# Performance work log

Hardware: AMD Instinct MI355X
Metric: run time of the kernel (lower is better)

## Reference

```python
import jax, jax.numpy as jnp
import numpy as np

B, L, HID, NH = 1, 2048, 3072, 24
HD = HID // NH          # 128
MLP = HID * 4           # 12288


def _layernorm(x, eps=1e-6):
    # LayerNorm without affine (pre_norm)
    mu = jnp.mean(x, axis=-1, keepdims=True)
    var = jnp.mean(jnp.square(x - mu), axis=-1, keepdims=True)
    return (x - mu) * jax.lax.rsqrt(var + eps)


def _rmsnorm(x, w):
    # torch.nn.RMSNorm with eps=None -> finfo(dtype).eps
    eps = jnp.finfo(x.dtype).eps
    ms = jnp.mean(jnp.square(x), axis=-1, keepdims=True)
    return x * jax.lax.rsqrt(ms + eps) * w


def _apply_rope(x, pe):
    # x: (B, L, H, D); pe: (B, 1, L, D//2, 2, 2)
    b, l, h, d = x.shape
    x_ = x.astype(jnp.float32).reshape(b, l, h, d // 2, 1, 2)
    f = pe[:, :, :, None]                       # (B,1,L,1,D//2,2,2)
    out = f[..., 0] * x_[..., 0] + f[..., 1] * x_[..., 1]
    return out.reshape(b, l, h, d).astype(x.dtype)


def setup_inputs() -> dict:
    key = jax.random.key(0)
    ks = jax.random.split(key, 16)
    s = 0.02
    # pe as proper 2x2 rotation matrices (EmbedND output structure)
    theta = jax.random.uniform(ks[0], (L, HD // 2), minval=0.0, maxval=2.0 * np.pi)
    cos, sin = jnp.cos(theta), jnp.sin(theta)
    rot = jnp.stack([jnp.stack([cos, -sin], -1), jnp.stack([sin, cos], -1)], -2)
    pe = rot[None, None].astype(jnp.float32)    # (1,1,L,HD//2,2,2)
    rnd = lambda k, shp: jax.random.normal(k, shp, jnp.float32)
    return {
        "x": rnd(ks[1], (B, L, HID)),
        "vec": rnd(ks[2], (B, HID)),
        "pe": pe,
        "w_mod": rnd(ks[3], (HID, 3 * HID)) * s,
        "b_mod": rnd(ks[4], (3 * HID,)) * s,
        "w_qkv": rnd(ks[5], (HID, 3 * HID)) * s,
        "b_qkv": rnd(ks[6], (3 * HID,)) * s,
        "w_fc1": rnd(ks[7], (HID, MLP)) * s,
        "b_fc1": rnd(ks[8], (MLP,)) * s,
        "w_fc2": rnd(ks[9], (MLP, HID)) * s,
        "b_fc2": rnd(ks[10], (HID,)) * s,
        "w_out": rnd(ks[11], (HID, HID)) * s,
        "b_out": rnd(ks[12], (HID,)) * s,
        "norm_q_w": jnp.ones((HD,), jnp.float32),
        "norm_k_w": jnp.ones((HD,), jnp.float32),
    }


def reference(x, vec, pe, w_mod, b_mod, w_qkv, b_qkv, w_fc1, b_fc1,
              w_fc2, b_fc2, w_out, b_out, norm_q_w, norm_k_w):
    # modulation: AWQ linear on silu(vec)
    mod = jax.nn.silu(vec) @ w_mod + b_mod            # (B, 3*HID)
    shift, scale, gate = jnp.split(mod[:, None, :], 3, axis=-1)
    x_mod = _layernorm(x) * (1.0 + scale) + shift      # (B, L, HID)

    # qkv projection (SVDQ linear, dequantized math == dense GEMM)
    qkv = x_mod @ w_qkv + b_qkv
    q, k, v = jnp.split(qkv, 3, axis=-1)
    q = _rmsnorm(q.reshape(B, L, NH, HD), norm_q_w)
    k = _rmsnorm(k.reshape(B, L, NH, HD), norm_k_w)
    q = _apply_rope(q, pe)
    k = _apply_rope(k, pe)
    v = v.reshape(B, L, NH, HD)

    # scaled dot-product attention
    scores = jnp.einsum("blhd,bmhd->bhlm", q, k) / jnp.sqrt(jnp.float32(HD))
    probs = jax.nn.softmax(scores, axis=-1)
    attn = jnp.einsum("bhlm,bmhd->blhd", probs, v).reshape(B, L, HID)

    # parallel MLP branch
    mlp = jax.nn.gelu(x_mod @ w_fc1 + b_fc1, approximate=True)
    mlp = mlp @ w_fc2 + b_fc2

    out = attn @ w_out + b_out + mlp
    return x + gate * out
```

## Files before the change

### kernel.cpp

```cpp
#include <hip/hip_runtime.h>
#include <hip/hip_bf16.h>
#include <stdint.h>


typedef __bf16 bf16;
typedef bf16 bf16x2 __attribute__((ext_vector_type(2)));
typedef bf16 bf16x4 __attribute__((ext_vector_type(4)));
typedef bf16 bf16x8 __attribute__((ext_vector_type(8)));
typedef float f32x4 __attribute__((ext_vector_type(4)));

#define L_SEQ 2048
#define HIDD  3072
#define NHH   24
#define HDD   128
#define MLPD  12288
#define N3Q   9216

struct PB { bf16* p[4]; };

__device__ __forceinline__ void gload_lds16(const bf16* g, bf16* l) {
  __builtin_amdgcn_global_load_lds(
      (const __attribute__((address_space(1))) unsigned int*)g,
      (__attribute__((address_space(3))) unsigned int*)l, 16, 0, 0);
}

__device__ __forceinline__ float gelu_tanh(float x) {
  float z = 0.7978845608028654f * (x + 0.044715f * x * x * x);
  float t = 1.f - 2.f / (__expf(2.f * z) + 1.f);
  return 0.5f * x * (1.f + t);
}

__global__ __launch_bounds__(256) void mod_partial(
    const float* __restrict__ vec, const float* __restrict__ w_mod,
    float* __restrict__ part) {
  __shared__ float sv[256];
  int y = blockIdx.y;
  int i0 = y * 256;
  {
    float xv = vec[i0 + threadIdx.x];
    sv[threadIdx.x] = xv / (1.f + __expf(-xv));
  }
  __syncthreads();
  int j = blockIdx.x * 256 + threadIdx.x;
  float acc = 0.f;
#pragma unroll 8
  for (int i = 0; i < 256; ++i)
    acc += sv[i] * w_mod[(size_t)(i0 + i) * N3Q + j];
  part[y * N3Q + j] = acc;
}

__global__ __launch_bounds__(256) void mod_reduce(
    const float* __restrict__ part, const float* __restrict__ b_mod,
    float* __restrict__ mod) {
  int j = blockIdx.x * 256 + threadIdx.x;
  float s = b_mod[j];
#pragma unroll
  for (int p = 0; p < 12; ++p) s += part[p * N3Q + j];
  mod[j] = s;
}

__global__ __launch_bounds__(256) void ln_mod_k(
    const float* __restrict__ x, const float* __restrict__ mod,
    bf16* __restrict__ xm) {
  __shared__ float sb[4];
  int l = blockIdx.x, t = threadIdx.x;
  const float* xr = x + (size_t)l * HIDD;
  float4 v[3];
  float s = 0.f;
#pragma unroll
  for (int p = 0; p < 3; ++p) {
    v[p] = *(const float4*)(xr + p * 1024 + t * 4);
    s += v[p].x + v[p].y + v[p].z + v[p].w;
  }
#pragma unroll
  for (int o = 32; o >= 1; o >>= 1) s += __shfl_xor(s, o);
  if (!(t & 63)) sb[t >> 6] = s;
  __syncthreads();
  float mean = (sb[0] + sb[1] + sb[2] + sb[3]) * (1.f / HIDD);
  __syncthreads();
  float vs = 0.f;
#pragma unroll
  for (int p = 0; p < 3; ++p) {
    float a = v[p].x - mean, b = v[p].y - mean, c = v[p].z - mean,
          d = v[p].w - mean;
    vs += a * a + b * b + c * c + d * d;
  }
#pragma unroll
  for (int o = 32; o >= 1; o >>= 1) vs += __shfl_xor(vs, o);
  if (!(t & 63)) sb[t >> 6] = vs;
  __syncthreads();
  float var = (sb[0] + sb[1] + sb[2] + sb[3]) * (1.f / HIDD);
  float rs = rsqrtf(var + 1e-6f);
#pragma unroll
  for (int p = 0; p < 3; ++p) {
    int j = p * 1024 + t * 4;
    float4 sc = *(const float4*)(mod + HIDD + j);
    float4 sh = *(const float4*)(mod + j);
    bf16x4 o;
    o[0] = (bf16)((v[p].x - mean) * rs * (1.f + sc.x) + sh.x);
    o[1] = (bf16)((v[p].y - mean) * rs * (1.f + sc.y) + sh.y);
    o[2] = (bf16)((v[p].z - mean) * rs * (1.f + sc.z) + sh.z);
    o[3] = (bf16)((v[p].w - mean) * rs * (1.f + sc.w) + sh.w);
    *(bf16x4*)(xm + (size_t)l * HIDD + j) = o;
  }
}

__global__ __launch_bounds__(256) void convT(
    const float* __restrict__ src, bf16* __restrict__ dst, int K, int N) {
  __shared__ bf16 tl[64 * 73];
  int n0 = blockIdx.x * 64, k0 = blockIdx.y * 64;
  int t = threadIdx.x;
#pragma unroll
  for (int p = 0; p < 4; ++p) {
    int idx = p * 256 + t;
    int kr = idx >> 4, c4 = (idx & 15) << 2;
    float4 v = *(const float4*)(src + (size_t)(k0 + kr) * N + n0 + c4);
    bf16x4 b;
    b[0] = (bf16)v.x; b[1] = (bf16)v.y; b[2] = (bf16)v.z; b[3] = (bf16)v.w;
    *(bf16x4*)(tl + kr * 73 + c4) = b;
  }
  __syncthreads();
#pragma unroll
  for (int p = 0; p < 2; ++p) {
    int idx = p * 256 + t;
    int nr = idx >> 3, c = idx & 7;
    bf16x8 o;
#pragma unroll
    for (int j = 0; j < 8; ++j) o[j] = tl[(c * 8 + j) * 73 + nr];
    *(bf16x8*)(dst + (size_t)(n0 + nr) * K + k0 + c * 8) = o;
  }
}

template <int EPI>
__global__ __launch_bounds__(512, 2) void gemm256(
    const bf16* __restrict__ A, const bf16* __restrict__ BT,
    const float* __restrict__ bias, int lda, int klen, int gy, int gz,
    PB dst, bf16* __restrict__ o1, const bf16* __restrict__ BT2,
    const bf16* __restrict__ BT3, float* __restrict__ o32) {
  __shared__ bf16 LA[2][2][8192];
  __shared__ bf16 LB[2][2][8192];
  const int tid = threadIdx.x;
  const int w = tid >> 6, lane = tid & 63;
  const int wm = w >> 2, wn = w & 3;
  const int g = lane >> 4, r16 = lane & 15;
  const int hb = wn >> 1, brow = (wn & 1) * 64;

  const int nwg = 8 * gy * gz;
  int id = (int)blockIdx.x;
  int sw = (id & 7) * (nwg >> 3) + (id >> 3);
  const int bx = sw & 7;
  const int rem = sw >> 3;
  const int by = rem % gy;
  const int bz = rem / gy;

  const int row0 = bx * 256, col0 = by * 256;

  const int s_r = tid >> 3, s_c = tid & 7;
  const int swzoff = (s_c ^ (s_r & 7)) << 3;

  int lda_eff = lda;
  const bf16* Abase = A;
  const bf16* Bbase = BT;
  size_t kb2 = 0;
  int bcol = col0;
  if (EPI == 2) {
    if (by >= 36)      { Bbase = BT3; bcol = col0 - 9216; }
    else if (by >= 32) { Bbase = BT2; bcol = col0 - 8192; }
  } else if (EPI == 3) {
    if (bz != 0) {
      lda_eff = MLPD;
      Abase = BT3;
      Bbase = BT2;
      kb2 = (size_t)(bz - 1) * 3072;
    }
  }
  const bf16* gA = Abase + (size_t)(row0 + s_r) * lda_eff + kb2 + swzoff;
  const bf16* gB = Bbase + (size_t)(bcol + s_r) * lda_eff + kb2 + swzoff;
  const int wofs = w * 512;

#define STG_A(buf, h, t)                                                       \
  do {                                                                         \
    gload_lds16(gA + (size_t)((h) * 128) * lda_eff + (size_t)(t) * 64,         \
                &LA[buf][h][wofs]);                                            \
    gload_lds16(gA + (size_t)((h) * 128 + 64) * lda_eff + (size_t)(t) * 64,    \
                &LA[buf][h][4096 + wofs]);                                     \
  } while (0)
#define STG_B(buf, h, t)                                                       \
  do {                                                                         \
    gload_lds16(gB + (size_t)((h) * 128) * lda_eff + (size_t)(t) * 64,         \
                &LB[buf][h][wofs]);                                            \
    gload_lds16(gB + (size_t)((h) * 128 + 64) * lda_eff + (size_t)(t) * 64,    \
                &LB[buf][h][4096 + wofs]);                                     \
  } while (0)
#define SB0() __builtin_amdgcn_sched_barrier(0)
#define RD_A4(DST, LAP, MB)                                                    \
  _Pragma("unroll") for (int m_ = 0; m_ < 4; ++m_)                             \
  _Pragma("unroll") for (int kk_ = 0; kk_ < 2; ++kk_)                          \
      DST[m_][kk_] = *(const bf16x8*)((LAP) + (((MB) + m_) * 16 + r16) * 64 +  \
                                      (((kk_ * 4 + g) ^ (r16 & 7)) << 3));
#define RD_B2(DST, LBP, NB)                                                    \
  _Pragma("unroll") for (int n_ = 0; n_ < 2; ++n_)                             \
  _Pragma("unroll") for (int kk_ = 0; kk_ < 2; ++kk_)                          \
      DST[n_][kk_] = *(const bf16x8*)(                                         \
          (LBP) + (brow + ((NB) + n_) * 16 + r16) * 64 +                       \
          (((kk_ * 4 + g) ^ (r16 & 7)) << 3));
#define QUAD(AF, BF, MB, NB)                                                   \
  do {                                                                         \
    __builtin_amdgcn_s_setprio(1);                                             \
    _Pragma("unroll") for (int kk_ = 0; kk_ < 2; ++kk_)                        \
    _Pragma("unroll") for (int m_ = 0; m_ < 4; ++m_)                           \
    _Pragma("unroll") for (int n_ = 0; n_ < 2; ++n_)                           \
        acc[(MB) + m_][(NB) + n_] = __builtin_amdgcn_mfma_f32_16x16x32_bf16(   \
            AF[m_][kk_], BF[n_][kk_], acc[(MB) + m_][(NB) + n_], 0, 0, 0);     \
    __builtin_amdgcn_s_setprio(0);                                             \
  } while (0)

#define GROUP(TB, T1, T2)                                                      \
  do {                                                                         \
    const bf16* la = &LA[TB][wm][0];                                           \
    const bf16* lb = &LB[TB][hb][0];                                           \
    bf16x8 aL[4][2], aH[4][2], bL[2][2], bH[2][2];                             \
                                           \
    RD_A4(aL, la, 0);                                                          \
    RD_B2(bL, lb, 0);                                                          \
    if ((T1) < nk) STG_B(TB ^ 1, 1, T1);                                       \
    __builtin_amdgcn_s_barrier();                                              \
    SB0();                                                                     \
    QUAD(aL, bL, 0, 0);                                                        \
    __builtin_amdgcn_s_barrier();                                              \
                      \
    RD_A4(aH, la, 4);                                                          \
    __builtin_amdgcn_s_barrier();                                              \
    SB0();                                                                     \
    QUAD(aH, bL, 4, 0);                                                        \
    __builtin_amdgcn_s_barrier();                                              \
     \
    RD_B2(bH, lb, 2);                                                          \
    if ((T2) < nk) { STG_A(TB, 0, T2); STG_A(TB, 1, T2); }                     \
    __builtin_amdgcn_s_barrier();                                              \
    SB0();                                                                     \
    QUAD(aL, bH, 0, 2);                                                        \
    __builtin_amdgcn_s_barrier();                                              \
       \
    if ((T2) < nk) {                                                           \
      STG_B(TB, 0, T2);                                                        \
      asm volatile("s_waitcnt vmcnt(6)" ::: "memory");                         \
    } else {                                                                   \
      asm volatile("s_waitcnt vmcnt(0)" ::: "memory");                         \
    }                                                                          \
    __builtin_amdgcn_s_barrier();                                              \
    SB0();                                                                     \
    QUAD(aH, bH, 4, 2);                                                        \
    __builtin_amdgcn_s_barrier();                                              \
  } while (0)

  f32x4 acc[8][4] = {};
  const int nk = klen >> 6;

  STG_A(0, 0, 0); STG_A(0, 1, 0); STG_B(0, 0, 0); STG_B(0, 1, 0);
  STG_A(1, 0, 1); STG_A(1, 1, 1); STG_B(1, 0, 1);
  asm volatile("s_waitcnt vmcnt(6)" ::: "memory");
  __builtin_amdgcn_s_barrier();

  for (int t = 0; t < nk; t += 2) {
    GROUP(0, t + 1, t + 2);
    GROUP(1, t + 2, t + 3);
  }
#undef STG_A
#undef STG_B
#undef SB0
#undef RD_A4
#undef RD_B2
#undef QUAD
#undef GROUP

  if (EPI == 2 && by < 36) {
    bf16* dp = dst.p[0];
#pragma unroll
    for (int m = 0; m < 8; ++m) {
      int row = row0 + wm * 128 + m * 16 + g * 4;
#pragma unroll
      for (int n = 0; n < 4; ++n) {
        int col = col0 + wn * 64 + n * 16 + r16;
#pragma unroll
        for (int r = 0; r < 4; ++r)
          dp[(size_t)(row + r) * N3Q + col] = (bf16)acc[m][n][r];
      }
    }
  } else if (EPI == 2) {
    bf16* dp = o1;
#pragma unroll
    for (int m = 0; m < 8; ++m) {
      int row = row0 + wm * 128 + m * 16 + g * 4;
#pragma unroll
      for (int n = 0; n < 4; ++n) {
        int col = col0 - 9216 + wn * 64 + n * 16 + r16;
        float bv = bias[col];
#pragma unroll
        for (int r = 0; r < 4; ++r)
          dp[(size_t)(row + r) * MLPD + col] = (bf16)gelu_tanh(acc[m][n][r] + bv);
      }
    }
  } else if (EPI == 3 && bz == 0) {
#pragma unroll
    for (int m = 0; m < 8; ++m) {
      int row = row0 + wm * 128 + m * 16 + g * 4;
#pragma unroll
      for (int n = 0; n < 4; ++n) {
        int col = col0 + wn * 64 + n * 16 + r16;
#pragma unroll
        for (int r = 0; r < 4; ++r)
          o32[(size_t)(row + r) * HIDD + col] = acc[m][n][r];
      }
    }
  } else {
    bf16* dp = dst.p[bz - 1];
#pragma unroll
    for (int m = 0; m < 8; ++m) {
      int row = row0 + wm * 128 + m * 16 + g * 4;
#pragma unroll
      for (int n = 0; n < 4; ++n) {
        int col = col0 + wn * 64 + n * 16 + r16;
#pragma unroll
        for (int r = 0; r < 4; ++r)
          dp[(size_t)(row + r) * HIDD + col] = (bf16)acc[m][n][r];
      }
    }
  }
}

__global__ __launch_bounds__(256) void qknorm_rope_k(
    const bf16* __restrict__ P, const float* __restrict__ b_qkv,
    const float* __restrict__ pe, const float* __restrict__ qw,
    const float* __restrict__ kw, bf16* __restrict__ qb,
    bf16* __restrict__ kb) {
  int t = threadIdx.x, lane = t & 63, w = t >> 6;
  int pair = blockIdx.x * 4 + w;
  int h = pair % NHH, l = pair / NHH;
  size_t qi = (size_t)l * N3Q + h * HDD + 2 * lane;
  size_t ob = (size_t)l * HIDD + h * HDD + 2 * lane;
  float4 f = *(const float4*)(pe + (size_t)l * 256 + lane * 4);
  float2 wq = *(const float2*)(qw + 2 * lane);
  float2 wk = *(const float2*)(kw + 2 * lane);
  {
    bf16x2 a = *(const bf16x2*)(P + qi);
    float2 bq = *(const float2*)(b_qkv + h * HDD + 2 * lane);
    float x0 = (float)a[0] + bq.x;
    float x1 = (float)a[1] + bq.y;
    float ss = x0 * x0 + x1 * x1;
#pragma unroll
    for (int o = 32; o >= 1; o >>= 1) ss += __shfl_xor(ss, o);
    float rs = rsqrtf(ss * (1.f / HDD) + 1.1920929e-7f);
    x0 *= rs * wq.x; x1 *= rs * wq.y;
    const float qs = 0.08838834764831845f;
    bf16x2 ov;
    ov[0] = (bf16)((f.x * x0 + f.y * x1) * qs);
    ov[1] = (bf16)((f.z * x0 + f.w * x1) * qs);
    *(bf16x2*)(qb + ob) = ov;
  }
  {
    bf16x2 a = *(const bf16x2*)(P + qi + HIDD);
    float2 bk = *(const float2*)(b_qkv + HIDD + h * HDD + 2 * lane);
    float x0 = (float)a[0] + bk.x;
    float x1 = (float)a[1] + bk.y;
    float ss = x0 * x0 + x1 * x1;
#pragma unroll
    for (int o = 32; o >= 1; o >>= 1) ss += __shfl_xor(ss, o);
    float rs = rsqrtf(ss * (1.f / HDD) + 1.1920929e-7f);
    x0 *= rs * wk.x; x1 *= rs * wk.y;
    bf16x2 ov;
    ov[0] = (bf16)(f.x * x0 + f.y * x1);
    ov[1] = (bf16)(f.z * x0 + f.w * x1);
    *(bf16x2*)(kb + ob) = ov;
  }
}

__global__ __launch_bounds__(256) void vtrans_k(
    const bf16* __restrict__ P, const float* __restrict__ b_qkv,
    bf16* __restrict__ vt) {
  __shared__ bf16 tl[128 * 128];
  int t = threadIdx.x, lt = blockIdx.x, h = blockIdx.y;
#pragma unroll
  for (int p = 0; p < 8; ++p) {
    int idx = p * 256 + t;
    int i = idx >> 4, c = idx & 15;
    size_t gi = (size_t)(lt * 128 + i) * N3Q + 2 * HIDD + h * HDD + c * 8;
    bf16x8 a = *(const bf16x8*)(P + gi);
    bf16x8 val;
#pragma unroll
    for (int e = 0; e < 8; ++e)
      val[e] = (bf16)((float)a[e] + b_qkv[2 * HIDD + h * HDD + c * 8 + e]);
    *(bf16x8*)(tl + i * 128 + ((c ^ (i & 15)) << 3)) = val;
  }
  __syncthreads();
#pragma unroll
  for (int p = 0; p < 8; ++p) {
    int idx = p * 256 + t;
    int j = idx >> 4, i8 = (idx & 15) << 3;
    bf16x8 o;
#pragma unroll
    for (int e = 0; e < 8; ++e) {
      int row = i8 + e;
      o[e] = tl[row * 128 + ((((j >> 3) ^ (row & 15)) << 3) | (j & 7))];
    }
    *(bf16x8*)(vt + ((size_t)h * HDD + j) * L_SEQ + lt * 128 + i8) = o;
  }
}

__global__ __launch_bounds__(256) void attn_k(
    const bf16* __restrict__ q, const bf16* __restrict__ k,
    const bf16* __restrict__ vt, bf16* __restrict__ out) {
  __shared__ bf16 Ks[64 * 128];
  __shared__ bf16 Vs[128 * 64];
  __shared__ bf16 Ps[4][16 * 72];
  int tid = threadIdx.x, lane = tid & 63, w = tid >> 6;
  int g = lane >> 4, r16 = lane & 15;
  int qt = blockIdx.x, h = blockIdx.y;
  int qbase = qt * 64 + w * 16;

  bf16x8 qreg[4];
  const bf16* qrow = q + (size_t)(qbase + r16) * HIDD + h * HDD;
#pragma unroll
  for (int c = 0; c < 4; ++c) qreg[c] = *(const bf16x8*)(qrow + c * 32 + g * 8);

  f32x4 acc[8] = {};
  float m_run = -3.0e38f, l_run = 0.f;
  bf16* ps = &Ps[w][0];

  for (int kv0 = 0; kv0 < L_SEQ; kv0 += 64) {
    __syncthreads();
#pragma unroll
    for (int p = 0; p < 4; ++p) {
      int ci = p * 256 + tid;
      {
        int rr = ci >> 4, cc = ci & 15;
        gload_lds16(k + (size_t)(kv0 + rr) * HIDD + h * HDD +
                        ((cc ^ (rr & 15)) << 3),
                    Ks + ((p * 4 + w) << 9));
      }
      {
        int rr = ci >> 3, cc = ci & 7;
        gload_lds16(vt + ((size_t)h * HDD + rr) * L_SEQ + kv0 +
                        ((cc ^ (rr & 7)) << 3),
                    Vs + ((p * 4 + w) << 9));
      }
    }
    __syncthreads();

    f32x4 st[4] = {};
#pragma unroll
    for (int m4 = 0; m4 < 4; ++m4) {
#pragma unroll
      for (int c = 0; c < 4; ++c) {
        int rr = m4 * 16 + r16;
        bf16x8 kf =
            *(const bf16x8*)(Ks + rr * 128 + (((c * 4 + g) ^ (rr & 15)) << 3));
        st[m4] =
            __builtin_amdgcn_mfma_f32_16x16x32_bf16(kf, qreg[c], st[m4], 0, 0, 0);
      }
    }
    float cmax = -3.0e38f;
#pragma unroll
    for (int m4 = 0; m4 < 4; ++m4)
#pragma unroll
      for (int r = 0; r < 4; ++r) cmax = fmaxf(cmax, st[m4][r]);
    cmax = fmaxf(cmax, __shfl_xor(cmax, 16));
    cmax = fmaxf(cmax, __shfl_xor(cmax, 32));
    float m_new = fmaxf(m_run, cmax);
    float corr = __expf(m_run - m_new);
    float psum = 0.f;
#pragma unroll
    for (int m4 = 0; m4 < 4; ++m4) {
      bf16x4 pk;
#pragma unroll
      for (int r = 0; r < 4; ++r) {
        float pv = __expf(st[m4][r] - m_new);
        psum += pv;
        pk[r] = (bf16)pv;
      }
      *(bf16x4*)(ps + r16 * 72 + m4 * 16 + g * 4) = pk;
    }
    psum += __shfl_xor(psum, 16);
    psum += __shfl_xor(psum, 32);
    l_run = l_run * corr + psum;
    m_run = m_new;
    float corr_r[4];
#pragma unroll
    for (int r = 0; r < 4; ++r) corr_r[r] = __shfl(corr, g * 4 + r);
#pragma unroll
    for (int nt = 0; nt < 8; ++nt)
#pragma unroll
      for (int r = 0; r < 4; ++r) acc[nt][r] *= corr_r[r];
#pragma unroll
    for (int ks = 0; ks < 2; ++ks) {
      bf16x8 pf = *(const bf16x8*)(ps + r16 * 72 + ks * 32 + g * 8);
#pragma unroll
      for (int nt = 0; nt < 8; ++nt) {
        int rr = nt * 16 + r16;
        bf16x8 vf =
            *(const bf16x8*)(Vs + rr * 64 + (((ks * 4 + g) ^ (rr & 7)) << 3));
        acc[nt] = __builtin_amdgcn_mfma_f32_16x16x32_bf16(pf, vf, acc[nt], 0, 0, 0);
      }
    }
  }
  float inv = 1.f / l_run;
  float inv_r[4];
#pragma unroll
  for (int r = 0; r < 4; ++r) inv_r[r] = __shfl(inv, g * 4 + r);
#pragma unroll
  for (int nt = 0; nt < 8; ++nt)
#pragma unroll
    for (int r = 0; r < 4; ++r)
      out[(size_t)(qbase + g * 4 + r) * HIDD + h * HDD + nt * 16 + r16] =
          (bf16)(acc[nt][r] * inv_r[r]);
}

__global__ __launch_bounds__(256) void final_k(
    const float* __restrict__ x, PB ps, const float* __restrict__ mod,
    const float* __restrict__ b_out, const float* __restrict__ b_fc2,
    float* __restrict__ out) {
  int l = blockIdx.x, t = threadIdx.x;
#pragma unroll
  for (int p = 0; p < 3; ++p) {
    int c = p * 1024 + t * 4;
    size_t idx = (size_t)l * HIDD + c;
    float4 xv = *(const float4*)(x + idx);
    float4 gv = *(const float4*)(mod + 2 * HIDD + c);
    float4 bo = *(const float4*)(b_out + c);
    float4 bf = *(const float4*)(b_fc2 + c);
    float4 da = *(const float4*)(out + idx);
    float a0 = da.x + bo.x + bf.x, a1 = da.y + bo.y + bf.y;
    float a2 = da.z + bo.z + bf.z, a3 = da.w + bo.w + bf.w;
#pragma unroll
    for (int i = 0; i < 4; ++i) {
      bf16x4 v = *(const bf16x4*)(ps.p[i] + idx);
      a0 += (float)v[0]; a1 += (float)v[1];
      a2 += (float)v[2]; a3 += (float)v[3];
    }
    float4 o;
    o.x = xv.x + gv.x * a0;
    o.y = xv.y + gv.y * a1;
    o.z = xv.z + gv.z * a2;
    o.w = xv.w + gv.w * a3;
    *(float4*)(out + idx) = o;
  }
}

extern "C" void kernel_launch(void* const* d_in, const int* in_sizes, int n_in,
                              void* d_out, int out_size, void* d_ws,
                              size_t ws_size, hipStream_t stream) {
  const float* x     = (const float*)d_in[0];
  const float* vec   = (const float*)d_in[1];
  const float* pe    = (const float*)d_in[2];
  const float* w_mod = (const float*)d_in[3];
  const float* b_mod = (const float*)d_in[4];
  const float* w_qkv = (const float*)d_in[5];
  const float* b_qkv = (const float*)d_in[6];
  const float* w_fc1 = (const float*)d_in[7];
  const float* b_fc1 = (const float*)d_in[8];
  const float* w_fc2 = (const float*)d_in[9];
  const float* b_fc2 = (const float*)d_in[10];
  const float* w_out = (const float*)d_in[11];
  const float* b_out = (const float*)d_in[12];
  const float* qw    = (const float*)d_in[13];
  const float* kw    = (const float*)d_in[14];
  float* out = (float*)d_out;

  char* ws = (char*)d_ws;
  float* mod  = (float*)(ws + 0);
  bf16* xmod  = (bf16*)(ws + 65536);
  bf16* qb    = (bf16*)(ws + 12648448);
  bf16* kbuf  = (bf16*)(ws + 25231360);
  bf16* vt    = (bf16*)(ws + 37814272);
  bf16* att   = (bf16*)(ws + 50397184);
  bf16* mlpF  = (bf16*)(ws + 62980096);
  bf16* wt    = (bf16*)(ws + 113311744);
  bf16* P0    = (bf16*)(ws + 188809216);
  float* part = (float*)(ws + 188809216);
  bf16* wtQlo = qb;
  bf16* wtScr = (bf16*)out;
  bf16* wtO   = P0;

  mod_partial<<<dim3(36, 12), 256, 0, stream>>>(vec, w_mod, part);
  mod_reduce<<<36, 256, 0, stream>>>(part, b_mod, mod);
  ln_mod_k<<<2048, 256, 0, stream>>>(x, mod, xmod);

  convT<<<dim3(128, 48), 256, 0, stream>>>(w_qkv, wtQlo, 3072, 9216);
  convT<<<dim3(16, 48), 256, 0, stream>>>(w_qkv + 8192, wtScr, 3072, 9216);
  convT<<<dim3(192, 48), 256, 0, stream>>>(w_fc1, wt, 3072, 12288);
  PB Pc = {}; Pc.p[0] = P0;
  gemm256<2><<<672, 512, 0, stream>>>(xmod, wtQlo, b_fc1, 3072, 3072, 84, 1,
                                      Pc, mlpF, wtScr, wt, nullptr);

  qknorm_rope_k<<<12288, 256, 0, stream>>>(P0, b_qkv, pe, qw, kw, qb, kbuf);
  vtrans_k<<<dim3(16, 24), 256, 0, stream>>>(P0, b_qkv, vt);
  attn_k<<<dim3(32, 24), 256, 0, stream>>>(qb, kbuf, vt, att);

  convT<<<dim3(48, 48), 256, 0, stream>>>(w_out, wtO, 3072, 3072);
  convT<<<dim3(48, 192), 256, 0, stream>>>(w_fc2, wt, 12288, 3072);
  PB Pf = {};
  Pf.p[0] = xmod; Pf.p[1] = qb; Pf.p[2] = kbuf; Pf.p[3] = vt;
  gemm256<3><<<480, 512, 0, stream>>>(att, wtO, nullptr, 3072, 3072, 12, 5,
                                      Pf, nullptr, wt, mlpF, out);

  final_k<<<2048, 256, 0, stream>>>(x, Pf, mod, b_out, b_fc2, out);
}
```

Before: 809.8 us.

## Fuse independent stages into combined launches to overlap weight transposes with compute

Merges the weight-transpose kernels with the modulation GEMV, the q/k norm+rope, the V transpose and the attention kernel into three heterogeneous launches, dispatching work by block index. This cuts launch count and lets bandwidth-bound transposes fill idle CUs, for example during the attention tail. In exchange, every block reserves the largest shared-memory footprint of its launch, which can reduce occupancy for the lightweight transpose blocks.

Result: no change. 811.5 us (+0.2%).

```diff
diff --git a/kernel.cpp b/kernel.cpp
--- a/kernel.cpp
+++ b/kernel.cpp
@@ -30,23 +30,285 @@
   return 0.5f * x * (1.f + t);
 }
 
-__global__ __launch_bounds__(256) void mod_partial(
+__device__ __forceinline__ void convT_tile(
+    const float* __restrict__ src, bf16* __restrict__ dst, int K, int N,
+    int bx, int by, bf16* tl) {
+  int n0 = bx * 64, k0 = by * 64;
+  int t = threadIdx.x;
+#pragma unroll
+  for (int p = 0; p < 4; ++p) {
+    int idx = p * 256 + t;
+    int kr = idx >> 4, c4 = (idx & 15) << 2;
+    float4 v = *(const float4*)(src + (size_t)(k0 + kr) * N + n0 + c4);
+    bf16x4 b;
+    b[0] = (bf16)v.x; b[1] = (bf16)v.y; b[2] = (bf16)v.z; b[3] = (bf16)v.w;
+    *(bf16x4*)(tl + kr * 73 + c4) = b;
+  }
+  __syncthreads();
+#pragma unroll
+  for (int p = 0; p < 2; ++p) {
+    int idx = p * 256 + t;
+    int nr = idx >> 3, c = idx & 7;
+    bf16x8 o;
+#pragma unroll
+    for (int j = 0; j < 8; ++j) o[j] = tl[(c * 8 + j) * 73 + nr];
+    *(bf16x8*)(dst + (size_t)(n0 + nr) * K + k0 + c * 8) = o;
+  }
+}
+
+__device__ __forceinline__ void mod_partial_body(
     const float* __restrict__ vec, const float* __restrict__ w_mod,
-    float* __restrict__ part) {
-  __shared__ float sv[256];
-  int y = blockIdx.y;
-  int i0 = y * 256;
+    float* __restrict__ part, int bx, int by, float* sv) {
+  int i0 = by * 256;
   {
     float xv = vec[i0 + threadIdx.x];
     sv[threadIdx.x] = xv / (1.f + __expf(-xv));
   }
   __syncthreads();
-  int j = blockIdx.x * 256 + threadIdx.x;
+  int j = bx * 256 + threadIdx.x;
   float acc = 0.f;
 #pragma unroll 8
   for (int i = 0; i < 256; ++i)
     acc += sv[i] * w_mod[(size_t)(i0 + i) * N3Q + j];
-  part[y * N3Q + j] = acc;
+  part[by * N3Q + j] = acc;
+}
+
+__device__ __forceinline__ void qknorm_body(
+    const bf16* __restrict__ P, const float* __restrict__ b_qkv,
+    const float* __restrict__ pe, const float* __restrict__ qw,
+    const float* __restrict__ kw, bf16* __restrict__ qb,
+    bf16* __restrict__ kb, int blk) {
+  int t = threadIdx.x, lane = t & 63, w = t >> 6;
+  int pair = blk * 4 + w;
+  int h = pair % NHH, l = pair / NHH;
+  size_t qi = (size_t)l * N3Q + h * HDD + 2 * lane;
+  size_t ob = (size_t)l * HIDD + h * HDD + 2 * lane;
+  float4 f = *(const float4*)(pe + (size_t)l * 256 + lane * 4);
+  float2 wq = *(const float2*)(qw + 2 * lane);
+  float2 wk = *(const float2*)(kw + 2 * lane);
+  {
+    bf16x2 a = *(const bf16x2*)(P + qi);
+    float2 bq = *(const float2*)(b_qkv + h * HDD + 2 * lane);
+    float x0 = (float)a[0] + bq.x;
+    float x1 = (float)a[1] + bq.y;
+    float ss = x0 * x0 + x1 * x1;
+#pragma unroll
+    for (int o = 32; o >= 1; o >>= 1) ss += __shfl_xor(ss, o);
+    float rs = rsqrtf(ss * (1.f / HDD) + 1.1920929e-7f);
+    x0 *= rs * wq.x; x1 *= rs * wq.y;
+    const float qs = 0.08838834764831845f;
+    bf16x2 ov;
+    ov[0] = (bf16)((f.x * x0 + f.y * x1) * qs);
+    ov[1] = (bf16)((f.z * x0 + f.w * x1) * qs);
+    *(bf16x2*)(qb + ob) = ov;
+  }
+  {
+    bf16x2 a = *(const bf16x2*)(P + qi + HIDD);
+    float2 bk = *(const float2*)(b_qkv + HIDD + h * HDD + 2 * lane);
+    float x0 = (float)a[0] + bk.x;
+    float x1 = (float)a[1] + bk.y;
+    float ss = x0 * x0 + x1 * x1;
+#pragma unroll
+    for (int o = 32; o >= 1; o >>= 1) ss += __shfl_xor(ss, o);
+    float rs = rsqrtf(ss * (1.f / HDD) + 1.1920929e-7f);
+    x0 *= rs * wk.x; x1 *= rs * wk.y;
+    bf16x2 ov;
+    ov[0] = (bf16)(f.x * x0 + f.y * x1);
+    ov[1] = (bf16)(f.z * x0 + f.w * x1);
+    *(bf16x2*)(kb + ob) = ov;
+  }
+}
+
+__device__ __forceinline__ void vtrans_body(
+    const bf16* __restrict__ P, const float* __restrict__ b_qkv,
+    bf16* __restrict__ vt, int lt, int h, bf16* tl) {
+  int t = threadIdx.x;
+#pragma unroll
+  for (int p = 0; p < 8; ++p) {
+    int idx = p * 256 + t;
+    int i = idx >> 4, c = idx & 15;
+    size_t gi = (size_t)(lt * 128 + i) * N3Q + 2 * HIDD + h * HDD + c * 8;
+    bf16x8 a = *(const bf16x8*)(P + gi);
+    bf16x8 val;
+#pragma unroll
+    for (int e = 0; e < 8; ++e)
+      val[e] = (bf16)((float)a[e] + b_qkv[2 * HIDD + h * HDD + c * 8 + e]);
+    *(bf16x8*)(tl + i * 128 + ((c ^ (i & 15)) << 3)) = val;
+  }
+  __syncthreads();
+#pragma unroll
+  for (int p = 0; p < 8; ++p) {
+    int idx = p * 256 + t;
+    int j = idx >> 4, i8 = (idx & 15) << 3;
+    bf16x8 o;
+#pragma unroll
+    for (int e = 0; e < 8; ++e) {
+      int row = i8 + e;
+      o[e] = tl[row * 128 + ((((j >> 3) ^ (row & 15)) << 3) | (j & 7))];
+    }
+    *(bf16x8*)(vt + ((size_t)h * HDD + j) * L_SEQ + lt * 128 + i8) = o;
+  }
+}
+
+__device__ __forceinline__ void attn_body(
+    const bf16* __restrict__ q, const bf16* __restrict__ k,
+    const bf16* __restrict__ vt, bf16* __restrict__ out, int qt, int h,
+    char* smem) {
+  bf16* Ks = (bf16*)smem;
+  bf16* Vs = (bf16*)(smem + 16384);
+  int tid = threadIdx.x, lane = tid & 63, w = tid >> 6;
+  int g = lane >> 4, r16 = lane & 15;
+  bf16* ps = (bf16*)(smem + 32768) + w * 1152;
+  int qbase = qt * 64 + w * 16;
+
+  bf16x8 qreg[4];
+  const bf16* qrow = q + (size_t)(qbase + r16) * HIDD + h * HDD;
+#pragma unroll
+  for (int c = 0; c < 4; ++c) qreg[c] = *(const bf16x8*)(qrow + c * 32 + g * 8);
+
+  f32x4 acc[8] = {};
+  float m_run = -3.0e38f, l_run = 0.f;
+
+  for (int kv0 = 0; kv0 < L_SEQ; kv0 += 64) {
+    __syncthreads();
+#pragma unroll
+    for (int p = 0; p < 4; ++p) {
+      int ci = p * 256 + tid;
+      {
+        int rr = ci >> 4, cc = ci & 15;
+        gload_lds16(k + (size_t)(kv0 + rr) * HIDD + h * HDD +
+                        ((cc ^ (rr & 15)) << 3),
+                    Ks + ((p * 4 + w) << 9));
+      }
+      {
+        int rr = ci >> 3, cc = ci & 7;
+        gload_lds16(vt + ((size_t)h * HDD + rr) * L_SEQ + kv0 +
+                        ((cc ^ (rr & 7)) << 3),
+                    Vs + ((p * 4 + w) << 9));
+      }
+    }
+    __syncthreads();
+
+    f32x4 st[4] = {};
+#pragma unroll
+    for (int m4 = 0; m4 < 4; ++m4) {
+#pragma unroll
+      for (int c = 0; c < 4; ++c) {
+        int rr = m4 * 16 + r16;
+        bf16x8 kf =
+            *(const bf16x8*)(Ks + rr * 128 + (((c * 4 + g) ^ (rr & 15)) << 3));
+        st[m4] =
+            __builtin_amdgcn_mfma_f32_16x16x32_bf16(kf, qreg[c], st[m4], 0, 0, 0);
+      }
+    }
+    float cmax = -3.0e38f;
+#pragma unroll
+    for (int m4 = 0; m4 < 4; ++m4)
+#pragma unroll
+      for (int r = 0; r < 4; ++r) cmax = fmaxf(cmax, st[m4][r]);
+    cmax = fmaxf(cmax, __shfl_xor(cmax, 16));
+    cmax = fmaxf(cmax, __shfl_xor(cmax, 32));
+    float m_new = fmaxf(m_run, cmax);
+    float corr = __expf(m_run - m_new);
+    float psum = 0.f;
+#pragma unroll
+    for (int m4 = 0; m4 < 4; ++m4) {
+      bf16x4 pk;
+#pragma unroll
+      for (int r = 0; r < 4; ++r) {
+        float pv = __expf(st[m4][r] - m_new);
+        psum += pv;
+        pk[r] = (bf16)pv;
+      }
+      *(bf16x4*)(ps + r16 * 72 + m4 * 16 + g * 4) = pk;
+    }
+    psum += __shfl_xor(psum, 16);
+    psum += __shfl_xor(psum, 32);
+    l_run = l_run * corr + psum;
+    m_run = m_new;
+    float corr_r[4];
+#pragma unroll
+    for (int r = 0; r < 4; ++r) corr_r[r] = __shfl(corr, g * 4 + r);
+#pragma unroll
+    for (int nt = 0; nt < 8; ++nt)
+#pragma unroll
+      for (int r = 0; r < 4; ++r) acc[nt][r] *= corr_r[r];
+#pragma unroll
+    for (int ks = 0; ks < 2; ++ks) {
+      bf16x8 pf = *(const bf16x8*)(ps + r16 * 72 + ks * 32 + g * 8);
+#pragma unroll
+      for (int nt = 0; nt < 8; ++nt) {
+        int rr = nt * 16 + r16;
+        bf16x8 vf =
+            *(const bf16x8*)(Vs + rr * 64 + (((ks * 4 + g) ^ (rr & 7)) << 3));
+        acc[nt] = __builtin_amdgcn_mfma_f32_16x16x32_bf16(pf, vf, acc[nt], 0, 0, 0);
+      }
+    }
+  }
+  float inv = 1.f / l_run;
+  float inv_r[4];
+#pragma unroll
+  for (int r = 0; r < 4; ++r) inv_r[r] = __shfl(inv, g * 4 + r);
+#pragma unroll
+  for (int nt = 0; nt < 8; ++nt)
+#pragma unroll
+    for (int r = 0; r < 4; ++r)
+      out[(size_t)(qbase + g * 4 + r) * HIDD + h * HDD + nt * 16 + r16] =
+          (bf16)(acc[nt][r] * inv_r[r]);
+}
+
+__global__ __launch_bounds__(256) void fused0(
+    const float* __restrict__ vec, const float* __restrict__ w_mod,
+    float* __restrict__ part, const float* __restrict__ w_qkv,
+    const float* __restrict__ w_fc1, bf16* __restrict__ wtQlo,
+    bf16* __restrict__ wtScr, bf16* __restrict__ wtG) {
+  __shared__ __align__(16) char smem[64 * 73 * 2];
+  int f = (int)blockIdx.x;
+  if (f < 9216) {
+    convT_tile(w_fc1, wtG, 3072, 12288, f % 192, f / 192, (bf16*)smem);
+  } else if (f < 15360) {
+    f -= 9216;
+    convT_tile(w_qkv, wtQlo, 3072, 9216, f % 128, f / 128, (bf16*)smem);
+  } else if (f < 16128) {
+    f -= 15360;
+    convT_tile(w_qkv + 8192, wtScr, 3072, 9216, f % 16, f / 16, (bf16*)smem);
+  } else {
+    f -= 16128;
+    mod_partial_body(vec, w_mod, part, f % 36, f / 36, (float*)smem);
+  }
+}
+
+__global__ __launch_bounds__(256) void fused1(
+    const float* __restrict__ w_fc2, bf16* __restrict__ wtG,
+    const bf16* __restrict__ P0, const float* __restrict__ b_qkv,
+    const float* __restrict__ pe, const float* __restrict__ qw,
+    const float* __restrict__ kw, bf16* __restrict__ qb,
+    bf16* __restrict__ kbuf, bf16* __restrict__ vt) {
+  __shared__ __align__(16) char smem[128 * 128 * 2];
+  int f = (int)blockIdx.x;
+  if (f < 9216) {
+    convT_tile(w_fc2, wtG, 12288, 3072, f % 48, f / 48, (bf16*)smem);
+  } else if (f < 9600) {
+    f -= 9216;
+    vtrans_body(P0, b_qkv, vt, f % 16, f / 16, (bf16*)smem);
+  } else {
+    f -= 9600;
+    qknorm_body(P0, b_qkv, pe, qw, kw, qb, kbuf, f);
+  }
+}
+
+__global__ __launch_bounds__(256) void fused2(
+    const bf16* __restrict__ qb, const bf16* __restrict__ kbuf,
+    const bf16* __restrict__ vt, bf16* __restrict__ att,
+    const float* __restrict__ w_out, bf16* __restrict__ wtO) {
+  __shared__ __align__(16) char smem[41984];
+  int f = (int)blockIdx.x;
+  if (f < 768) {
+    attn_body(qb, kbuf, vt, att, f & 31, f >> 5, smem);
+  } else {
+    f -= 768;
+    convT_tile(w_out, wtO, 3072, 3072, f % 48, f / 48, (bf16*)smem);
+  }
 }
 
 __global__ __launch_bounds__(256) void mod_reduce(
@@ -102,32 +364,6 @@
     o[2] = (bf16)((v[p].z - mean) * rs * (1.f + sc.z) + sh.z);
     o[3] = (bf16)((v[p].w - mean) * rs * (1.f + sc.w) + sh.w);
     *(bf16x4*)(xm + (size_t)l * HIDD + j) = o;
-  }
-}
-
-__global__ __launch_bounds__(256) void convT(
-    const float* __restrict__ src, bf16* __restrict__ dst, int K, int N) {
-  __shared__ bf16 tl[64 * 73];
-  int n0 = blockIdx.x * 64, k0 = blockIdx.y * 64;
-  int t = threadIdx.x;
-#pragma unroll
-  for (int p = 0; p < 4; ++p) {
-    int idx = p * 256 + t;
-    int kr = idx >> 4, c4 = (idx & 15) << 2;
-    float4 v = *(const float4*)(src + (size_t)(k0 + kr) * N + n0 + c4);
-    bf16x4 b;
-    b[0] = (bf16)v.x; b[1] = (bf16)v.y; b[2] = (bf16)v.z; b[3] = (bf16)v.w;
-    *(bf16x4*)(tl + kr * 73 + c4) = b;
-  }
-  __syncthreads();
-#pragma unroll
-  for (int p = 0; p < 2; ++p) {
-    int idx = p * 256 + t;
-    int nr = idx >> 3, c = idx & 7;
-    bf16x8 o;
-#pragma unroll
-    for (int j = 0; j < 8; ++j) o[j] = tl[(c * 8 + j) * 73 + nr];
-    *(bf16x8*)(dst + (size_t)(n0 + nr) * K + k0 + c * 8) = o;
   }
 }
 
@@ -329,192 +565,6 @@
   }
 }
 
-__global__ __launch_bounds__(256) void qknorm_rope_k(
-    const bf16* __restrict__ P, const float* __restrict__ b_qkv,
-    const float* __restrict__ pe, const float* __restrict__ qw,
-    const float* __restrict__ kw, bf16* __restrict__ qb,
-    bf16* __restrict__ kb) {
-  int t = threadIdx.x, lane = t & 63, w = t >> 6;
-  int pair = blockIdx.x * 4 + w;
-  int h = pair % NHH, l = pair / NHH;
-  size_t qi = (size_t)l * N3Q + h * HDD + 2 * lane;
-  size_t ob = (size_t)l * HIDD + h * HDD + 2 * lane;
-  float4 f = *(const float4*)(pe + (size_t)l * 256 + lane * 4);
-  float2 wq = *(const float2*)(qw + 2 * lane);
-  float2 wk = *(const float2*)(kw + 2 * lane);
-  {
-    bf16x2 a = *(const bf16x2*)(P + qi);
-    float2 bq = *(const float2*)(b_qkv + h * HDD + 2 * lane);
-    float x0 = (float)a[0] + bq.x;
-    float x1 = (float)a[1] + bq.y;
-    float ss = x0 * x0 + x1 * x1;
-#pragma unroll
-    for (int o = 32; o >= 1; o >>= 1) ss += __shfl_xor(ss, o);
-    float rs = rsqrtf(ss * (1.f / HDD) + 1.1920929e-7f);
-    x0 *= rs * wq.x; x1 *= rs * wq.y;
-    const float qs = 0.08838834764831845f;
-    bf16x2 ov;
-    ov[0] = (bf16)((f.x * x0 + f.y * x1) * qs);
-    ov[1] = (bf16)((f.z * x0 + f.w * x1) * qs);
-    *(bf16x2*)(qb + ob) = ov;
-  }
-  {
-    bf16x2 a = *(const bf16x2*)(P + qi + HIDD);
-    float2 bk = *(const float2*)(b_qkv + HIDD + h * HDD + 2 * lane);
-    float x0 = (float)a[0] + bk.x;
-    float x1 = (float)a[1] + bk.y;
-    float ss = x0 * x0 + x1 * x1;
-#pragma unroll
-    for (int o = 32; o >= 1; o >>= 1) ss += __shfl_xor(ss, o);
-    float rs = rsqrtf(ss * (1.f / HDD) + 1.1920929e-7f);
-    x0 *= rs * wk.x; x1 *= rs * wk.y;
-    bf16x2 ov;
-    ov[0] = (bf16)(f.x * x0 + f.y * x1);
-    ov[1] = (bf16)(f.z * x0 + f.w * x1);
-    *(bf16x2*)(kb + ob) = ov;
-  }
-}
-
-__global__ __launch_bounds__(256) void vtrans_k(
-    const bf16* __restrict__ P, const float* __restrict__ b_qkv,
-    bf16* __restrict__ vt) {
-  __shared__ bf16 tl[128 * 128];
-  int t = threadIdx.x, lt = blockIdx.x, h = blockIdx.y;
-#pragma unroll
-  for (int p = 0; p < 8; ++p) {
-    int idx = p * 256 + t;
-    int i = idx >> 4, c = idx & 15;
-    size_t gi = (size_t)(lt * 128 + i) * N3Q + 2 * HIDD + h * HDD + c * 8;
-    bf16x8 a = *(const bf16x8*)(P + gi);
-    bf16x8 val;
-#pragma unroll
-    for (int e = 0; e < 8; ++e)
-      val[e] = (bf16)((float)a[e] + b_qkv[2 * HIDD + h * HDD + c * 8 + e]);
-    *(bf16x8*)(tl + i * 128 + ((c ^ (i & 15)) << 3)) = val;
-  }
-  __syncthreads();
-#pragma unroll
-  for (int p = 0; p < 8; ++p) {
-    int idx = p * 256 + t;
-    int j = idx >> 4, i8 = (idx & 15) << 3;
-    bf16x8 o;
-#pragma unroll
-    for (int e = 0; e < 8; ++e) {
-      int row = i8 + e;
-      o[e] = tl[row * 128 + ((((j >> 3) ^ (row & 15)) << 3) | (j & 7))];
-    }
-    *(bf16x8*)(vt + ((size_t)h * HDD + j) * L_SEQ + lt * 128 + i8) = o;
-  }
-}
-
-__global__ __launch_bounds__(256) void attn_k(
-    const bf16* __restrict__ q, const bf16* __restrict__ k,
-    const bf16* __restrict__ vt, bf16* __restrict__ out) {
-  __shared__ bf16 Ks[64 * 128];
-  __shared__ bf16 Vs[128 * 64];
-  __shared__ bf16 Ps[4][16 * 72];
-  int tid = threadIdx.x, lane = tid & 63, w = tid >> 6;
-  int g = lane >> 4, r16 = lane & 15;
-  int qt = blockIdx.x, h = blockIdx.y;
-  int qbase = qt * 64 + w * 16;
-
-  bf16x8 qreg[4];
-  const bf16* qrow = q + (size_t)(qbase + r16) * HIDD + h * HDD;
-#pragma unroll
-  for (int c = 0; c < 4; ++c) qreg[c] = *(const bf16x8*)(qrow + c * 32 + g * 8);
-
-  f32x4 acc[8] = {};
-  float m_run = -3.0e38f, l_run = 0.f;
-  bf16* ps = &Ps[w][0];
-
-  for (int kv0 = 0; kv0 < L_SEQ; kv0 += 64) {
-    __syncthreads();
-#pragma unroll
-    for (int p = 0; p < 4; ++p) {
-      int ci = p * 256 + tid;
-      {
-        int rr = ci >> 4, cc = ci & 15;
-        gload_lds16(k + (size_t)(kv0 + rr) * HIDD + h * HDD +
-                        ((cc ^ (rr & 15)) << 3),
-                    Ks + ((p * 4 + w) << 9));
-      }
-      {
-        int rr = ci >> 3, cc = ci & 7;
-        gload_lds16(vt + ((size_t)h * HDD + rr) * L_SEQ + kv0 +
-                        ((cc ^ (rr & 7)) << 3),
-                    Vs + ((p * 4 + w) << 9));
-      }
-    }
-    __syncthreads();
-
-    f32x4 st[4] = {};
-#pragma unroll
-    for (int m4 = 0; m4 < 4; ++m4) {
-#pragma unroll
-      for (int c = 0; c < 4; ++c) {
-        int rr = m4 * 16 + r16;
-        bf16x8 kf =
-            *(const bf16x8*)(Ks + rr * 128 + (((c * 4 + g) ^ (rr & 15)) << 3));
-        st[m4] =
-            __builtin_amdgcn_mfma_f32_16x16x32_bf16(kf, qreg[c], st[m4], 0, 0, 0);
-      }
-    }
-    float cmax = -3.0e38f;
-#pragma unroll
-    for (int m4 = 0; m4 < 4; ++m4)
-#pragma unroll
-      for (int r = 0; r < 4; ++r) cmax = fmaxf(cmax, st[m4][r]);
-    cmax = fmaxf(cmax, __shfl_xor(cmax, 16));
-    cmax = fmaxf(cmax, __shfl_xor(cmax, 32));
-    float m_new = fmaxf(m_run, cmax);
-    float corr = __expf(m_run - m_new);
-    float psum = 0.f;
-#pragma unroll
-    for (int m4 = 0; m4 < 4; ++m4) {
-      bf16x4 pk;
-#pragma unroll
-      for (int r = 0; r < 4; ++r) {
-        float pv = __expf(st[m4][r] - m_new);
-        psum += pv;
-        pk[r] = (bf16)pv;
-      }
-      *(bf16x4*)(ps + r16 * 72 + m4 * 16 + g * 4) = pk;
-    }
-    psum += __shfl_xor(psum, 16);
-    psum += __shfl_xor(psum, 32);
-    l_run = l_run * corr + psum;
-    m_run = m_new;
-    float corr_r[4];
-#pragma unroll
-    for (int r = 0; r < 4; ++r) corr_r[r] = __shfl(corr, g * 4 + r);
-#pragma unroll
-    for (int nt = 0; nt < 8; ++nt)
-#pragma unroll
-      for (int r = 0; r < 4; ++r) acc[nt][r] *= corr_r[r];
-#pragma unroll
-    for (int ks = 0; ks < 2; ++ks) {
-      bf16x8 pf = *(const bf16x8*)(ps + r16 * 72 + ks * 32 + g * 8);
-#pragma unroll
-      for (int nt = 0; nt < 8; ++nt) {
-        int rr = nt * 16 + r16;
-        bf16x8 vf =
-            *(const bf16x8*)(Vs + rr * 64 + (((ks * 4 + g) ^ (rr & 7)) << 3));
-        acc[nt] = __builtin_amdgcn_mfma_f32_16x16x32_bf16(pf, vf, acc[nt], 0, 0, 0);
-      }
-    }
-  }
-  float inv = 1.f / l_run;
-  float inv_r[4];
-#pragma unroll
-  for (int r = 0; r < 4; ++r) inv_r[r] = __shfl(inv, g * 4 + r);
-#pragma unroll
-  for (int nt = 0; nt < 8; ++nt)
-#pragma unroll
-    for (int r = 0; r < 4; ++r)
-      out[(size_t)(qbase + g * 4 + r) * HIDD + h * HDD + nt * 16 + r16] =
-          (bf16)(acc[nt][r] * inv_r[r]);
-}
-
 __global__ __launch_bounds__(256) void final_k(
     const float* __restrict__ x, PB ps, const float* __restrict__ mod,
     const float* __restrict__ b_out, const float* __restrict__ b_fc2,
@@ -581,23 +631,20 @@
   bf16* wtScr = (bf16*)out;
   bf16* wtO   = P0;
 
-  mod_partial<<<dim3(36, 12), 256, 0, stream>>>(vec, w_mod, part);
+  fused0<<<16560, 256, 0, stream>>>(vec, w_mod, part, w_qkv, w_fc1, wtQlo,
+                                    wtScr, wt);
   mod_reduce<<<36, 256, 0, stream>>>(part, b_mod, mod);
   ln_mod_k<<<2048, 256, 0, stream>>>(x, mod, xmod);
 
-  convT<<<dim3(128, 48), 256, 0, stream>>>(w_qkv, wtQlo, 3072, 9216);
-  convT<<<dim3(16, 48), 256, 0, stream>>>(w_qkv + 8192, wtScr, 3072, 9216);
-  convT<<<dim3(192, 48), 256, 0, stream>>>(w_fc1, wt, 3072, 12288);
   PB Pc = {}; Pc.p[0] = P0;
   gemm256<2><<<672, 512, 0, stream>>>(xmod, wtQlo, b_fc1, 3072, 3072, 84, 1,
                                       Pc, mlpF, wtScr, wt, nullptr);
 
-  qknorm_rope_k<<<12288, 256, 0, stream>>>(P0, b_qkv, pe, qw, kw, qb, kbuf);
-  vtrans_k<<<dim3(16, 24), 256, 0, stream>>>(P0, b_qkv, vt);
-  attn_k<<<dim3(32, 24), 256, 0, stream>>>(qb, kbuf, vt, att);
-
-  convT<<<dim3(48, 48), 256, 0, stream>>>(w_out, wtO, 3072, 3072);
-  convT<<<dim3(48, 192), 256, 0, stream>>>(w_fc2, wt, 12288, 3072);
+  fused1<<<21888, 256, 0, stream>>>(w_fc2, wt, P0, b_qkv, pe, qw, kw, qb,
+                                    kbuf, vt);
+
+  fused2<<<3072, 256, 0, stream>>>(qb, kbuf, vt, att, w_out, wtO);
+
   PB Pf = {};
   Pf.p[0] = xmod; Pf.p[1] = qb; Pf.p[2] = kbuf; Pf.p[3] = vt;
   gemm256<3><<<480, 512, 0, stream>>>(att, wtO, nullptr, 3072, 3072, 12, 5,
```
